# Kernel tuning notes

Measured on AMD Instinct MI355X. Metric: run time of the kernel, lower is better.

Reference implementation:

```python
import jax, jax.numpy as jnp
import numpy as np

N_NODES = 10000
N_EDGES = 160000
F_IN, D, DEPTH, F_OUT = 6, 512, 10, 1


def setup_inputs() -> dict:
    key = jax.random.key(0)
    ks = jax.random.split(key, 10)
    features = jax.random.normal(ks[0], (N_NODES, F_IN), dtype=jnp.float32)
    src = jax.random.randint(ks[1], (N_EDGES,), 0, N_NODES, dtype=jnp.int32)
    dst = jax.random.randint(ks[2], (N_EDGES,), 0, N_NODES, dtype=jnp.int32)
    s_in = 1.0 / np.sqrt(F_IN)
    s_h = 1.0 / np.sqrt(D)
    W_in = jax.random.uniform(ks[3], (F_IN, D), jnp.float32, -s_in, s_in)
    b_in = jax.random.uniform(ks[4], (D,), jnp.float32, -s_in, s_in)
    Ws = jax.random.uniform(ks[5], (DEPTH, D, D), jnp.float32, -s_h, s_h)
    bs = jax.random.uniform(ks[6], (DEPTH, D), jnp.float32, -s_h, s_h)
    W_out = jax.random.uniform(ks[7], (D, F_OUT), jnp.float32, -s_h, s_h)
    b_out = jax.random.uniform(ks[8], (F_OUT,), jnp.float32, -s_h, s_h)
    return {"features": features, "W_in": W_in, "b_in": b_in, "Ws": Ws,
            "bs": bs, "W_out": W_out, "b_out": b_out, "src": src, "dst": dst}


def reference(features, W_in, b_in, Ws, bs, W_out, b_out, src, dst):
    n = features.shape[0]
    # GCNLayer: aggregate = scatter-sum of neighbor features (copy_src + sum), then Linear
    agg = jax.ops.segment_sum(features[src], dst, num_segments=n)  # [N, F_in]
    x = jax.nn.relu(agg @ W_in + b_in)  # ReLU only after input layer (per forward)

    def step(x, wb):
        W, b = wb
        a = jax.ops.segment_sum(x[src], dst, num_segments=n)  # [N, D]
        return a @ W + b, None  # no activation between hidden GCN layers

    x, _ = jax.lax.scan(step, x, (Ws, bs))
    return x @ W_out + b_out  # [N, 1]
```

## Files before the change

kernel.cpp:

```cpp
#include <hip/hip_runtime.h>

#define N_NODES 10000
#define N_EDGES 160000
#define DVAL    512
#define DEPTH   10



__global__ void zero_int_kernel(int* p, int n) {
    int i = blockIdx.x * 256 + threadIdx.x;
    if (i < n) p[i] = 0;
}

__global__ void count_deg_kernel(const int* __restrict__ dst, int* __restrict__ deg, int n) {
    int i = blockIdx.x * 256 + threadIdx.x;
    if (i < n) atomicAdd(&deg[dst[i]], 1);
}

__global__ __launch_bounds__(1024) void scan_kernel(const int* __restrict__ deg,
                                                    int* __restrict__ row_ptr,
                                                    int* __restrict__ cursor) {
    __shared__ int sums[1024];
    const int tid = threadIdx.x;
    const int CH = 10;
    int base = tid * CH;
    int local[CH];
    int s = 0;
#pragma unroll
    for (int i = 0; i < CH; i++) {
        int idx = base + i;
        int v = (idx < N_NODES) ? deg[idx] : 0;
        local[i] = s;
        s += v;
    }
    sums[tid] = s;
    __syncthreads();
    for (int off = 1; off < 1024; off <<= 1) {
        int v = (tid >= off) ? sums[tid - off] : 0;
        __syncthreads();
        sums[tid] += v;
        __syncthreads();
    }
    int chunk_base = (tid > 0) ? sums[tid - 1] : 0;
#pragma unroll
    for (int i = 0; i < CH; i++) {
        int idx = base + i;
        if (idx < N_NODES) {
            int v = chunk_base + local[i];
            row_ptr[idx] = v;
            cursor[idx] = v;
        }
    }
    if (tid == 1023) row_ptr[N_NODES] = sums[1023];
}

__global__ void fill_edges_kernel(const int* __restrict__ src, const int* __restrict__ dst,
                                  int* __restrict__ cursor, int* __restrict__ esrc, int n) {
    int i = blockIdx.x * 256 + threadIdx.x;
    if (i < n) {
        int p = atomicAdd(&cursor[dst[i]], 1);
        esrc[p] = src[i];
    }
}

__global__ __launch_bounds__(256) void matvec_gamma_kernel(const float* __restrict__ W,
                                                           const float* __restrict__ b,
                                                           const float* __restrict__ v_in,
                                                           float* __restrict__ v_out,
                                                           float* __restrict__ gamma_slot) {
    const int gw = (blockIdx.x * 256 + threadIdx.x) >> 6;
    const int lane = threadIdx.x & 63;
    {
        const float* row = W + (size_t)gw * 512;
        float s = 0.f;
#pragma unroll
        for (int c = 0; c < 8; c++) s += row[lane + c * 64] * v_in[lane + c * 64];
#pragma unroll
        for (int off = 32; off > 0; off >>= 1) s += __shfl_down(s, off, 64);
        if (lane == 0) v_out[gw] = s;
    }
    if (gw == 511) {
        float s = 0.f;
#pragma unroll
        for (int c = 0; c < 8; c++) s += b[lane + c * 64] * v_in[lane + c * 64];
#pragma unroll
        for (int off = 32; off > 0; off >>= 1) s += __shfl_down(s, off, 64);
        if (lane == 0) *gamma_slot = s;
    }
}

__global__ __launch_bounds__(256) void aggregate6_kernel(const float* __restrict__ feat,
                                                         const int* __restrict__ row_ptr,
                                                         const int* __restrict__ esrc,
                                                         float* __restrict__ agg6) {
    int t = blockIdx.x * 256 + threadIdx.x;
    int node = t >> 3;
    int c = t & 7;
    if (node >= N_NODES || c >= 6) return;
    int start = row_ptr[node], end = row_ptr[node + 1];
    float a0 = 0.f, a1 = 0.f;
    int e = start;
    for (; e + 2 <= end; e += 2) {
        a0 += feat[esrc[e] * 6 + c];
        a1 += feat[esrc[e + 1] * 6 + c];
    }
    if (e < end) a0 += feat[esrc[e] * 6 + c];
    agg6[node * 6 + c] = a0 + a1;
}

__global__ __launch_bounds__(256) void input_z_kernel(const float* __restrict__ agg6,
                                                      const float* __restrict__ W_in,
                                                      const float* __restrict__ b_in,
                                                      const float* __restrict__ vtilde,
                                                      float* __restrict__ z) {
    __shared__ float red[4];
    const int node = blockIdx.x;
    const int j = threadIdx.x;
    const int lane = j & 63;
    const int wave = j >> 6;
    float a[6];
#pragma unroll
    for (int k = 0; k < 6; k++) a[k] = agg6[node * 6 + k];
    float s = 0.f;
#pragma unroll
    for (int r = 0; r < 2; r++) {
        int jj = j + r * 256;
        float t = b_in[jj];
#pragma unroll
        for (int k = 0; k < 6; k++) t += a[k] * W_in[k * 512 + jj];
        s += fmaxf(t, 0.f) * vtilde[jj];
    }
#pragma unroll
    for (int off = 32; off > 0; off >>= 1) s += __shfl_down(s, off, 64);
    if (lane == 0) red[wave] = s;
    __syncthreads();
    if (j == 0) z[node] = (red[0] + red[1]) + (red[2] + red[3]);
}

__global__ __launch_bounds__(256) void col_agg_kernel(const float* __restrict__ r_in,
                                                      const int* __restrict__ row_ptr,
                                                      const int* __restrict__ esrc,
                                                      const float* __restrict__ gamma,
                                                      int gi,
                                                      const float* __restrict__ b_out,
                                                      int is_last,
                                                      float* __restrict__ r_out) {
    int i = blockIdx.x * 256 + threadIdx.x;
    if (i >= N_NODES) return;
    int s = row_ptr[i], e = row_ptr[i + 1];
    float a0 = 0.f, a1 = 0.f, a2 = 0.f, a3 = 0.f;
    int p = s;
    for (; p + 4 <= e; p += 4) {
        int i0 = esrc[p], i1 = esrc[p + 1], i2 = esrc[p + 2], i3 = esrc[p + 3];
        a0 += r_in[i0];
        a1 += r_in[i1];
        a2 += r_in[i2];
        a3 += r_in[i3];
    }
    for (; p < e; p++) a0 += r_in[esrc[p]];
    float res = (a0 + a1) + (a2 + a3) + gamma[gi];
    if (is_last) res += b_out[0];
    r_out[i] = res;
}


extern "C" void kernel_launch(void* const* d_in, const int* in_sizes, int n_in,
                              void* d_out, int out_size, void* d_ws, size_t ws_size,
                              hipStream_t stream) {
    const float* features = (const float*)d_in[0];
    const float* W_in     = (const float*)d_in[1];
    const float* b_in     = (const float*)d_in[2];
    const float* Ws       = (const float*)d_in[3];
    const float* bs       = (const float*)d_in[4];
    const float* W_out    = (const float*)d_in[5];
    const float* b_out    = (const float*)d_in[6];
    const int*   src      = (const int*)d_in[7];
    const int*   dst      = (const int*)d_in[8];
    float* out = (float*)d_out;

    char* p = (char*)d_ws;
    auto alloc = [&](size_t bytes) {
        char* r = p;
        p += (bytes + 255) & ~size_t(255);
        return r;
    };
    int* deg     = (int*)alloc((size_t)N_NODES * 4);
    int* row_ptr = (int*)alloc((size_t)(N_NODES + 1) * 4);
    int* cursor  = (int*)alloc((size_t)N_NODES * 4);
    int* esrc    = (int*)alloc((size_t)N_EDGES * 4);
    float* agg6  = (float*)alloc((size_t)N_NODES * 6 * 4);
    float* v_a   = (float*)alloc(512 * 4);
    float* v_b   = (float*)alloc(512 * 4);
    float* gamma = (float*)alloc(DEPTH * 4);
    float* r_a   = (float*)alloc((size_t)N_NODES * 4);
    float* r_b   = (float*)alloc((size_t)N_NODES * 4);

    zero_int_kernel<<<(N_NODES + 255) / 256, 256, 0, stream>>>(deg, N_NODES);
    count_deg_kernel<<<(N_EDGES + 255) / 256, 256, 0, stream>>>(dst, deg, N_EDGES);
    scan_kernel<<<1, 1024, 0, stream>>>(deg, row_ptr, cursor);
    fill_edges_kernel<<<(N_EDGES + 255) / 256, 256, 0, stream>>>(src, dst, cursor, esrc, N_EDGES);

    hipMemcpyAsync(v_a, W_out, 512 * sizeof(float), hipMemcpyDeviceToDevice, stream);
    float* v_cur = v_a;
    float* v_nxt = v_b;
    for (int l = DEPTH - 1; l >= 0; l--) {
        matvec_gamma_kernel<<<128, 256, 0, stream>>>(Ws + (size_t)l * 512 * 512,
                                                     bs + (size_t)l * 512,
                                                     v_cur, v_nxt, gamma + l);
        float* t = v_cur; v_cur = v_nxt; v_nxt = t;
    }

    aggregate6_kernel<<<(N_NODES * 8 + 255) / 256, 256, 0, stream>>>(features, row_ptr, esrc, agg6);
    input_z_kernel<<<N_NODES, 256, 0, stream>>>(agg6, W_in, b_in, v_cur, r_a);

    float* r_cur = r_a;
    float* r_nxt = r_b;
    for (int l = 0; l < DEPTH; l++) {
        int last = (l == DEPTH - 1);
        col_agg_kernel<<<(N_NODES + 255) / 256, 256, 0, stream>>>(
            r_cur, row_ptr, esrc, gamma, l, b_out, last, last ? out : r_nxt);
        float* t = r_cur; r_cur = r_nxt; r_nxt = t;
    }
}
```

Baseline: 194.2 us.

## Fuse whole GCN pipeline into one persistent kernel with grid barriers

Replaces about 27 separate kernel launches (CSR build, backward matvec chain, input projection, 10 scalar aggregations) with a single 80-block persistent kernel that uses software grid barriers between phases. The W_out back-propagation matvec chain is spread across the CSR-build and aggregation phases so it overlaps with graph work. The input projection is packed into an interleaved weight table, and each node is handled by two threads. This is meant to remove launch and inter-kernel gaps. The cost is relying on all 80 blocks being co-resident for the spin barriers, and each barrier adds its own sync cost.

```diff
diff --git a/kernel.cpp b/kernel.cpp
--- a/kernel.cpp
+++ b/kernel.cpp
@@ -1,166 +1,205 @@
 #include <hip/hip_runtime.h>
+
 
 #define N_NODES 10000
 #define N_EDGES 160000
-#define DVAL    512
 #define DEPTH   10
 
-
-
-__global__ void zero_int_kernel(int* p, int n) {
-    int i = blockIdx.x * 256 + threadIdx.x;
-    if (i < n) p[i] = 0;
-}
-
-__global__ void count_deg_kernel(const int* __restrict__ dst, int* __restrict__ deg, int n) {
-    int i = blockIdx.x * 256 + threadIdx.x;
-    if (i < n) atomicAdd(&deg[dst[i]], 1);
-}
-
-__global__ __launch_bounds__(1024) void scan_kernel(const int* __restrict__ deg,
-                                                    int* __restrict__ row_ptr,
-                                                    int* __restrict__ cursor) {
-    __shared__ int sums[1024];
-    const int tid = threadIdx.x;
-    const int CH = 10;
-    int base = tid * CH;
-    int local[CH];
-    int s = 0;
-#pragma unroll
-    for (int i = 0; i < CH; i++) {
-        int idx = base + i;
-        int v = (idx < N_NODES) ? deg[idx] : 0;
-        local[i] = s;
-        s += v;
-    }
-    sums[tid] = s;
+#define NB      80
+#define NTH     (NB * 256)
+#define NWAVES  (NTH / 64)
+#define RWAVES  (NWAVES - 4)
+
+__device__ __forceinline__ void gbar(int* cnt, int* gen, int phase) {
     __syncthreads();
-    for (int off = 1; off < 1024; off <<= 1) {
-        int v = (tid >= off) ? sums[tid - off] : 0;
+    if (threadIdx.x == 0) {
+        __threadfence();
+        int prev = __hip_atomic_fetch_add(cnt, 1, __ATOMIC_ACQ_REL,
+                                          __HIP_MEMORY_SCOPE_AGENT);
+        if (prev == NB * (phase + 1) - 1) {
+            __hip_atomic_store(gen, phase + 1, __ATOMIC_RELEASE,
+                               __HIP_MEMORY_SCOPE_AGENT);
+        } else {
+            while (__hip_atomic_load(gen, __ATOMIC_RELAXED,
+                                     __HIP_MEMORY_SCOPE_AGENT) < phase + 1)
+                __builtin_amdgcn_s_sleep(1);
+        }
+        __threadfence();
+    }
+    __syncthreads();
+}
+
+__device__ __forceinline__ void chain_step(int s, int gw, int lane,
+                                           const float* __restrict__ Ws,
+                                           const float* __restrict__ bs,
+                                           const float* __restrict__ W_out,
+                                           float* __restrict__ vbufs,
+                                           float* __restrict__ gamma) {
+    if (gw < 4) return;
+    const int l = 9 - s;
+    const float* vin = (s == 0) ? W_out : (vbufs + (s & 1) * 512);
+    float* vout = vbufs + ((s + 1) & 1) * 512;
+    const float* W = Ws + (size_t)l * 512 * 512;
+    const int w = gw - 4;
+#pragma unroll
+    for (int rr = 0; rr < 2; rr++) {
+        int row = w + RWAVES * rr;
+        if (row < 512) {
+            const float* Wr = W + (size_t)row * 512;
+            float acc = 0.f;
+#pragma unroll
+            for (int c = 0; c < 8; c++) acc += Wr[lane + 64 * c] * vin[lane + 64 * c];
+#pragma unroll
+            for (int off = 32; off; off >>= 1) acc += __shfl_xor(acc, off, 64);
+            if (lane == 0) vout[row] = acc;
+        }
+    }
+    if (gw == 255) {
+        const float* bl = bs + (size_t)l * 512;
+        float acc = 0.f;
+#pragma unroll
+        for (int c = 0; c < 8; c++) acc += bl[lane + 64 * c] * vin[lane + 64 * c];
+#pragma unroll
+        for (int off = 32; off; off >>= 1) acc += __shfl_xor(acc, off, 64);
+        if (lane == 0) gamma[l] = acc;
+    }
+}
+
+extern "C" __global__ void __launch_bounds__(256, 1) gcn_mega(
+    const float* __restrict__ features, const float* __restrict__ W_in,
+    const float* __restrict__ b_in, const float* __restrict__ Ws,
+    const float* __restrict__ bs, const float* __restrict__ W_out,
+    const float* __restrict__ b_out, const int* __restrict__ src,
+    const int* __restrict__ dst, float* __restrict__ out,
+    int* bar_cnt, int* bar_gen, int* deg, int* row_ptr, int* cursor,
+    int* esrc, float* vbufs, float* gamma, float* Wb,
+    float* rb0, float* rb1)
+{
+    const int t    = blockIdx.x * 256 + threadIdx.x;
+    const int gw   = t >> 6;
+    const int lane = t & 63;
+    int bp = 0;
+
+    for (int e = t; e < N_EDGES; e += NTH) atomicAdd(&deg[dst[e]], 1);
+    if (blockIdx.x == 0) {
+        for (int idx = threadIdx.x; idx < 4096; idx += 256) {
+            int j = idx >> 3, k = idx & 7;
+            float v = 0.f;
+            if (k < 6) v = W_in[k * 512 + j];
+            else if (k == 6) v = b_in[j];
+            Wb[idx] = v;
+        }
+    }
+    chain_step(0, gw, lane, Ws, bs, W_out, vbufs, gamma);
+    gbar(bar_cnt, bar_gen, bp); bp++;
+
+    if (blockIdx.x == 0) {
+        __shared__ int sums[256];
+        const int tt = threadIdx.x;
+        const int base = tt * 40;
+        int ssum = 0;
+#pragma unroll 8
+        for (int i = 0; i < 40; i++) {
+            int idx = base + i;
+            ssum += (idx < N_NODES) ? deg[idx] : 0;
+        }
+        sums[tt] = ssum;
         __syncthreads();
-        sums[tid] += v;
-        __syncthreads();
-    }
-    int chunk_base = (tid > 0) ? sums[tid - 1] : 0;
-#pragma unroll
-    for (int i = 0; i < CH; i++) {
-        int idx = base + i;
-        if (idx < N_NODES) {
-            int v = chunk_base + local[i];
-            row_ptr[idx] = v;
-            cursor[idx] = v;
-        }
-    }
-    if (tid == 1023) row_ptr[N_NODES] = sums[1023];
-}
-
-__global__ void fill_edges_kernel(const int* __restrict__ src, const int* __restrict__ dst,
-                                  int* __restrict__ cursor, int* __restrict__ esrc, int n) {
-    int i = blockIdx.x * 256 + threadIdx.x;
-    if (i < n) {
-        int p = atomicAdd(&cursor[dst[i]], 1);
-        esrc[p] = src[i];
-    }
-}
-
-__global__ __launch_bounds__(256) void matvec_gamma_kernel(const float* __restrict__ W,
-                                                           const float* __restrict__ b,
-                                                           const float* __restrict__ v_in,
-                                                           float* __restrict__ v_out,
-                                                           float* __restrict__ gamma_slot) {
-    const int gw = (blockIdx.x * 256 + threadIdx.x) >> 6;
-    const int lane = threadIdx.x & 63;
-    {
-        const float* row = W + (size_t)gw * 512;
-        float s = 0.f;
-#pragma unroll
-        for (int c = 0; c < 8; c++) s += row[lane + c * 64] * v_in[lane + c * 64];
-#pragma unroll
-        for (int off = 32; off > 0; off >>= 1) s += __shfl_down(s, off, 64);
-        if (lane == 0) v_out[gw] = s;
-    }
-    if (gw == 511) {
-        float s = 0.f;
-#pragma unroll
-        for (int c = 0; c < 8; c++) s += b[lane + c * 64] * v_in[lane + c * 64];
-#pragma unroll
-        for (int off = 32; off > 0; off >>= 1) s += __shfl_down(s, off, 64);
-        if (lane == 0) *gamma_slot = s;
-    }
-}
-
-__global__ __launch_bounds__(256) void aggregate6_kernel(const float* __restrict__ feat,
-                                                         const int* __restrict__ row_ptr,
-                                                         const int* __restrict__ esrc,
-                                                         float* __restrict__ agg6) {
-    int t = blockIdx.x * 256 + threadIdx.x;
-    int node = t >> 3;
-    int c = t & 7;
-    if (node >= N_NODES || c >= 6) return;
-    int start = row_ptr[node], end = row_ptr[node + 1];
-    float a0 = 0.f, a1 = 0.f;
-    int e = start;
-    for (; e + 2 <= end; e += 2) {
-        a0 += feat[esrc[e] * 6 + c];
-        a1 += feat[esrc[e + 1] * 6 + c];
-    }
-    if (e < end) a0 += feat[esrc[e] * 6 + c];
-    agg6[node * 6 + c] = a0 + a1;
-}
-
-__global__ __launch_bounds__(256) void input_z_kernel(const float* __restrict__ agg6,
-                                                      const float* __restrict__ W_in,
-                                                      const float* __restrict__ b_in,
-                                                      const float* __restrict__ vtilde,
-                                                      float* __restrict__ z) {
-    __shared__ float red[4];
-    const int node = blockIdx.x;
-    const int j = threadIdx.x;
-    const int lane = j & 63;
-    const int wave = j >> 6;
-    float a[6];
-#pragma unroll
-    for (int k = 0; k < 6; k++) a[k] = agg6[node * 6 + k];
-    float s = 0.f;
-#pragma unroll
-    for (int r = 0; r < 2; r++) {
-        int jj = j + r * 256;
-        float t = b_in[jj];
-#pragma unroll
-        for (int k = 0; k < 6; k++) t += a[k] * W_in[k * 512 + jj];
-        s += fmaxf(t, 0.f) * vtilde[jj];
-    }
-#pragma unroll
-    for (int off = 32; off > 0; off >>= 1) s += __shfl_down(s, off, 64);
-    if (lane == 0) red[wave] = s;
-    __syncthreads();
-    if (j == 0) z[node] = (red[0] + red[1]) + (red[2] + red[3]);
-}
-
-__global__ __launch_bounds__(256) void col_agg_kernel(const float* __restrict__ r_in,
-                                                      const int* __restrict__ row_ptr,
-                                                      const int* __restrict__ esrc,
-                                                      const float* __restrict__ gamma,
-                                                      int gi,
-                                                      const float* __restrict__ b_out,
-                                                      int is_last,
-                                                      float* __restrict__ r_out) {
-    int i = blockIdx.x * 256 + threadIdx.x;
-    if (i >= N_NODES) return;
-    int s = row_ptr[i], e = row_ptr[i + 1];
-    float a0 = 0.f, a1 = 0.f, a2 = 0.f, a3 = 0.f;
-    int p = s;
-    for (; p + 4 <= e; p += 4) {
-        int i0 = esrc[p], i1 = esrc[p + 1], i2 = esrc[p + 2], i3 = esrc[p + 3];
-        a0 += r_in[i0];
-        a1 += r_in[i1];
-        a2 += r_in[i2];
-        a3 += r_in[i3];
-    }
-    for (; p < e; p++) a0 += r_in[esrc[p]];
-    float res = (a0 + a1) + (a2 + a3) + gamma[gi];
-    if (is_last) res += b_out[0];
-    r_out[i] = res;
+        for (int off = 1; off < 256; off <<= 1) {
+            int v = (tt >= off) ? sums[tt - off] : 0;
+            __syncthreads();
+            sums[tt] += v;
+            __syncthreads();
+        }
+        int run = (tt > 0) ? sums[tt - 1] : 0;
+        for (int i = 0; i < 40; i++) {
+            int idx = base + i;
+            if (idx < N_NODES) {
+                row_ptr[idx] = run;
+                cursor[idx]  = run;
+                run += deg[idx];
+            }
+        }
+        if (tt == 255) row_ptr[N_NODES] = run;
+    }
+    chain_step(1, gw, lane, Ws, bs, W_out, vbufs, gamma);
+    gbar(bar_cnt, bar_gen, bp); bp++;
+
+    for (int e = t; e < N_EDGES; e += NTH) {
+        int d = dst[e];
+        int pos = atomicAdd(&cursor[d], 1);
+        esrc[pos] = src[e];
+    }
+    chain_step(2, gw, lane, Ws, bs, W_out, vbufs, gamma);
+    gbar(bar_cnt, bar_gen, bp); bp++;
+
+    const int node = t >> 1;
+    const int half = t & 1;
+    int ns = 0, ne = 0;
+    float a0 = 0.f, a1 = 0.f, a2 = 0.f, a3 = 0.f, a4 = 0.f, a5 = 0.f;
+    if (node < N_NODES) {
+        ns = row_ptr[node];
+        ne = row_ptr[node + 1];
+        for (int pp = ns + half; pp < ne; pp += 2) {
+            int j = esrc[pp];
+            const float2* f = (const float2*)(features + (size_t)j * 6);
+            float2 f0 = f[0], f1 = f[1], f2 = f[2];
+            a0 += f0.x; a1 += f0.y; a2 += f1.x;
+            a3 += f1.y; a4 += f2.x; a5 += f2.y;
+        }
+        a0 += __shfl_xor(a0, 1, 64);
+        a1 += __shfl_xor(a1, 1, 64);
+        a2 += __shfl_xor(a2, 1, 64);
+        a3 += __shfl_xor(a3, 1, 64);
+        a4 += __shfl_xor(a4, 1, 64);
+        a5 += __shfl_xor(a5, 1, 64);
+    }
+    chain_step(3, gw, lane, Ws, bs, W_out, vbufs, gamma);
+    gbar(bar_cnt, bar_gen, bp); bp++;
+
+    for (int s = 4; s <= 9; s++) {
+        chain_step(s, gw, lane, Ws, bs, W_out, vbufs, gamma);
+        gbar(bar_cnt, bar_gen, bp); bp++;
+    }
+
+    if (node < N_NODES) {
+        const float4* Wb4 = (const float4*)Wb;
+        const float* vt = vbufs;
+        float zacc = 0.f;
+#pragma unroll 4
+        for (int jj = 0; jj < 256; jj++) {
+            int j = (jj << 1) | half;
+            float4 wA = Wb4[2 * j];
+            float4 wB = Wb4[2 * j + 1];
+            float tv = wB.z + a0 * wA.x + a1 * wA.y + a2 * wA.z +
+                       a3 * wA.w + a4 * wB.x + a5 * wB.y;
+            zacc += fmaxf(tv, 0.f) * vt[j];
+        }
+        zacc += __shfl_xor(zacc, 1, 64);
+        if (half == 0) rb0[node] = zacc;
+    }
+    gbar(bar_cnt, bar_gen, bp); bp++;
+
+    for (int l = 0; l < DEPTH; l++) {
+        if (node < N_NODES) {
+            const float* rin = (l & 1) ? rb1 : rb0;
+            float h0 = 0.f, h1 = 0.f;
+            int pp = ns + half;
+            for (; pp + 2 < ne; pp += 4) {
+                h0 += rin[esrc[pp]];
+                h1 += rin[esrc[pp + 2]];
+            }
+            if (pp < ne) h0 += rin[esrc[pp]];
+            float hs = h0 + h1;
+            hs += __shfl_xor(hs, 1, 64);
+            if (half == 0) {
+                float res = hs + gamma[l];
+                if (l == DEPTH - 1) out[node] = res + b_out[0];
+                else ((l & 1) ? rb0 : rb1)[node] = res;
+            }
+        }
+        if (l < DEPTH - 1) { gbar(bar_cnt, bar_gen, bp); bp++; }
+    }
 }
 
 
@@ -178,47 +217,23 @@
     const int*   dst      = (const int*)d_in[8];
     float* out = (float*)d_out;
 
-    char* p = (char*)d_ws;
-    auto alloc = [&](size_t bytes) {
-        char* r = p;
-        p += (bytes + 255) & ~size_t(255);
-        return r;
-    };
-    int* deg     = (int*)alloc((size_t)N_NODES * 4);
-    int* row_ptr = (int*)alloc((size_t)(N_NODES + 1) * 4);
-    int* cursor  = (int*)alloc((size_t)N_NODES * 4);
-    int* esrc    = (int*)alloc((size_t)N_EDGES * 4);
-    float* agg6  = (float*)alloc((size_t)N_NODES * 6 * 4);
-    float* v_a   = (float*)alloc(512 * 4);
-    float* v_b   = (float*)alloc(512 * 4);
-    float* gamma = (float*)alloc(DEPTH * 4);
-    float* r_a   = (float*)alloc((size_t)N_NODES * 4);
-    float* r_b   = (float*)alloc((size_t)N_NODES * 4);
-
-    zero_int_kernel<<<(N_NODES + 255) / 256, 256, 0, stream>>>(deg, N_NODES);
-    count_deg_kernel<<<(N_EDGES + 255) / 256, 256, 0, stream>>>(dst, deg, N_EDGES);
-    scan_kernel<<<1, 1024, 0, stream>>>(deg, row_ptr, cursor);
-    fill_edges_kernel<<<(N_EDGES + 255) / 256, 256, 0, stream>>>(src, dst, cursor, esrc, N_EDGES);
-
-    hipMemcpyAsync(v_a, W_out, 512 * sizeof(float), hipMemcpyDeviceToDevice, stream);
-    float* v_cur = v_a;
-    float* v_nxt = v_b;
-    for (int l = DEPTH - 1; l >= 0; l--) {
-        matvec_gamma_kernel<<<128, 256, 0, stream>>>(Ws + (size_t)l * 512 * 512,
-                                                     bs + (size_t)l * 512,
-                                                     v_cur, v_nxt, gamma + l);
-        float* t = v_cur; v_cur = v_nxt; v_nxt = t;
-    }
-
-    aggregate6_kernel<<<(N_NODES * 8 + 255) / 256, 256, 0, stream>>>(features, row_ptr, esrc, agg6);
-    input_z_kernel<<<N_NODES, 256, 0, stream>>>(agg6, W_in, b_in, v_cur, r_a);
-
-    float* r_cur = r_a;
-    float* r_nxt = r_b;
-    for (int l = 0; l < DEPTH; l++) {
-        int last = (l == DEPTH - 1);
-        col_agg_kernel<<<(N_NODES + 255) / 256, 256, 0, stream>>>(
-            r_cur, row_ptr, esrc, gamma, l, b_out, last, last ? out : r_nxt);
-        float* t = r_cur; r_cur = r_nxt; r_nxt = t;
-    }
-}
+    char* base = (char*)d_ws;
+    int*   bar_cnt = (int*)(base + 0);
+    int*   bar_gen = (int*)(base + 64);
+    int*   deg     = (int*)(base + 128);
+    int*   row_ptr = (int*)(base + 40192);
+    int*   cursor  = (int*)(base + 80256);
+    int*   esrc    = (int*)(base + 120320);
+    float* vbufs   = (float*)(base + 760320);
+    float* gamma   = (float*)(base + 764416);
+    float* Wb      = (float*)(base + 764480);
+    float* rb0     = (float*)(base + 780864);
+    float* rb1     = (float*)(base + 820928);
+
+    hipMemsetAsync(base, 0, 40128, stream);
+
+    gcn_mega<<<NB, 256, 0, stream>>>(features, W_in, b_in, Ws, bs, W_out, b_out,
+                                     src, dst, out,
+                                     bar_cnt, bar_gen, deg, row_ptr, cursor,
+                                     esrc, vbufs, gamma, Wb, rb0, rb1);
+}
```

Result: slower. 336.5 us (+73.3%).
